# Optimization experiments

Measured on AMD Instinct MI355X. Metric: run time of the kernel, lower is better.

The kernel has to match this reference:

```python
import jax, jax.numpy as jnp
import numpy as np


def _conv1x1(x, w, b):
    # x: (B,C_in,H,W), w: (C_out,C_in), b: (C_out,)
    return jnp.einsum('bchw,oc->bohw', x, w) + b[None, :, None, None]


def _maxpool2x2(x):
    B, C, H, W = x.shape
    return x.reshape(B, C, H // 2, 2, W // 2, 2).max(axis=(3, 5))


def setup_inputs() -> dict:
    key = jax.random.key(0)
    ks = jax.random.split(key, 10)
    B, C, H, W = 16, 64, 64, 64
    d8, d2 = C // 8, C // 2
    s = 0.05
    return {
        'x': jax.random.normal(ks[0], (B, C, H, W), dtype=jnp.float32),
        'w_theta': jax.random.normal(ks[1], (d8, C), dtype=jnp.float32) * s,
        'b_theta': jnp.zeros((d8,), dtype=jnp.float32),
        'w_phi': jax.random.normal(ks[2], (d8, C), dtype=jnp.float32) * s,
        'b_phi': jnp.zeros((d8,), dtype=jnp.float32),
        'w_g': jax.random.normal(ks[3], (d2, C), dtype=jnp.float32) * s,
        'b_g': jnp.zeros((d2,), dtype=jnp.float32),
        'w_o': jax.random.normal(ks[4], (C, d2), dtype=jnp.float32) * s,
        'b_o': jnp.zeros((C,), dtype=jnp.float32),
        'sigma': jnp.ones((1,), dtype=jnp.float32),
    }


def reference(x, w_theta, b_theta, w_phi, b_phi, w_g, b_g, w_o, b_o, sigma):
    B, C, H, W = x.shape
    N = H * W
    theta = _conv1x1(x, w_theta, b_theta).reshape(B, C // 8, N)            # (B, d8, N)
    phi = _maxpool2x2(_conv1x1(x, w_phi, b_phi)).reshape(B, C // 8, N // 4)  # (B, d8, N/4)
    attn = jax.nn.softmax(jnp.einsum('bdn,bdm->bnm', theta, phi), axis=-1)   # (B, N, N/4)
    g = _maxpool2x2(_conv1x1(x, w_g, b_g)).reshape(B, C // 2, N // 4)        # (B, d2, N/4)
    attn_g = jnp.einsum('bcm,bnm->bcn', g, attn).reshape(B, C // 2, H, W)
    attn_g = _conv1x1(attn_g, w_o, b_o)
    return x + sigma[0] * attn_g
```

## Files before the change

kernel.cpp:

```cpp
#include <hip/hip_runtime.h>


#define B_   16
#define C_   64
#define HW_  4096
#define M_   1024

typedef __attribute__((ext_vector_type(8))) short bf16x8;
typedef __attribute__((ext_vector_type(4))) float f32x4;
typedef __attribute__((ext_vector_type(4))) _Float16 f16x4;

#define LOG2E 1.44269504088896340736f

__device__ __forceinline__ unsigned short f2bf(float f) {
    union { float f; unsigned int u; } v; v.f = f;
    return (unsigned short)((v.u + 0x7FFFu + ((v.u >> 16) & 1u)) >> 16);
}
__device__ __forceinline__ unsigned int packh2(float a, float b) {
    auto h = __builtin_amdgcn_cvt_pkrtz(a, b);
    union { decltype(h) h; unsigned int u; } v;
    v.h = h;
    return v.u;
}
__device__ __forceinline__ unsigned int pack2t(float a, float b) {
    union { float f; unsigned int u; } ua, ub; ua.f = a; ub.f = b;
    return (ua.u >> 16) | (ub.u & 0xFFFF0000u);
}

__global__ __launch_bounds__(256) void proj_kernel(
    const float* __restrict__ x,
    const float* __restrict__ w_theta, const float* __restrict__ b_theta,
    const float* __restrict__ w_phi,   const float* __restrict__ b_phi,
    const float* __restrict__ w_g,     const float* __restrict__ b_g,
    unsigned short* __restrict__ thetaH,
    unsigned short* __restrict__ phiH,
    unsigned short* __restrict__ gTp)
{
    __shared__ __align__(16) float x_l[64 * 132];
    __shared__ float pool_l[128][41];

    const int tid = threadIdx.x;
    const int b   = blockIdx.y;
    const int rp  = blockIdx.x;
    const int n0  = rp * 128;

    {
        const float4* src = (const float4*)(x + (size_t)b * C_ * HW_ + n0);
        #pragma unroll
        for (int j = 0; j < 8; j++) {
            int idx = tid + j * 256;
            int c = idx >> 5, p4 = idx & 31;
            float4 v = src[(size_t)c * (HW_ / 4) + p4];
            *(float4*)&x_l[c * 132 + p4 * 4] = v;
        }
    }
    __syncthreads();

    const int px = tid & 127;
    const int og = tid >> 7;

    if (og == 0) {
        float th[8], ph[8], g0[8];
        #pragma unroll
        for (int o = 0; o < 8; o++) { th[o] = b_theta[o]; ph[o] = b_phi[o]; g0[o] = b_g[o]; }
        #pragma unroll 4
        for (int c = 0; c < C_; c++) {
            float xv = x_l[c * 132 + px];
            #pragma unroll
            for (int o = 0; o < 8; o++) th[o] += xv * w_theta[o * 64 + c];
            #pragma unroll
            for (int o = 0; o < 8; o++) ph[o] += xv * w_phi[o * 64 + c];
            #pragma unroll
            for (int o = 0; o < 8; o++) g0[o] += xv * w_g[o * 64 + c];
        }
        unsigned short* tout = thetaH + ((size_t)b * HW_ + n0 + px) * 8;
        uint4 tv;
        tv.x = packh2(th[0] * LOG2E, th[1] * LOG2E);
        tv.y = packh2(th[2] * LOG2E, th[3] * LOG2E);
        tv.z = packh2(th[4] * LOG2E, th[5] * LOG2E);
        tv.w = packh2(th[6] * LOG2E, th[7] * LOG2E);
        *(uint4*)tout = tv;
        #pragma unroll
        for (int o = 0; o < 8; o++) { pool_l[px][o] = ph[o]; pool_l[px][8 + o] = g0[o]; }
    } else {
        float gg[24];
        #pragma unroll
        for (int o = 0; o < 24; o++) gg[o] = b_g[8 + o];
        #pragma unroll 4
        for (int c = 0; c < C_; c++) {
            float xv = x_l[c * 132 + px];
            #pragma unroll
            for (int o = 0; o < 24; o++) gg[o] += xv * w_g[(8 + o) * 64 + c];
        }
        #pragma unroll
        for (int o = 0; o < 24; o++) pool_l[px][16 + o] = gg[o];
    }
    __syncthreads();

    {
        const int j   = tid & 31;
        const int grp = tid >> 5;
        const int p00 = 2 * j, p01 = 2 * j + 1, p10 = 64 + 2 * j, p11 = 65 + 2 * j;
        const int mq   = rp * 32 + j;
        const int pcol = rp * 32 + ((j >> 2) & 3) * 8 + (j >> 4) * 4 + (j & 3);
        #pragma unroll
        for (int k = 0; k < 5; k++) {
            const int ch = grp * 5 + k;
            float v = fmaxf(fmaxf(pool_l[p00][ch], pool_l[p01][ch]),
                            fmaxf(pool_l[p10][ch], pool_l[p11][ch]));
            if (ch < 8)
                ((_Float16*)phiH)[((size_t)b * M_ + mq) * 16 + ch] = (_Float16)v;
            else
                gTp[((size_t)b * 32 + (ch - 8)) * M_ + pcol] = f2bf(v);
        }
        if (tid < 32) {
            *(uint4*)((_Float16*)phiH + ((size_t)b * M_ + rp * 32 + tid) * 16 + 8) =
                make_uint4(0, 0, 0, 0);
        }
    }
}

__global__ __launch_bounds__(256, 4) void attn_kernel(
    const float* __restrict__ x,
    const unsigned short* __restrict__ thetaH,
    const unsigned short* __restrict__ phiH,
    const unsigned short* __restrict__ gTp,
    const float* __restrict__ w_o, const float* __restrict__ b_o,
    const float* __restrict__ sigma,
    float* __restrict__ out)
{
    __shared__ float Op_l[4][32 * 33];
    __shared__ float rs_l[4][32];

    const int tid   = threadIdx.x;
    const int b     = blockIdx.y;
    const int qbase = blockIdx.x * 32;
    const int wv    = tid >> 6;
    const int lane  = tid & 63;
    const int ln15  = lane & 15;
    const int quad  = lane >> 4;

    const _Float16* phiP = (const _Float16*)phiH + (size_t)b * M_ * 16;
    const unsigned short* gP = gTp + (size_t)b * 32 * M_;

    f16x4 th[2];
    {
        const f16x4 z = {0, 0, 0, 0};
        #pragma unroll
        for (int qt = 0; qt < 2; qt++) {
            const _Float16* tp = (const _Float16*)thetaH
                + ((size_t)b * HW_ + qbase + qt * 16 + ln15) * 8 + (quad & 1) * 4;
            f16x4 t = *(const f16x4*)tp;
            th[qt] = (quad < 2) ? t : z;
        }
    }

    #define LD_PHI(ch_, mt_) \
        (*(const f16x4*)(phiP + ((ch_) * 64 + (mt_) * 16 + ln15) * 16 + quad * 4))
    #define LD_G(ch_, h_, s_) \
        (*(const bf16x8*)(gP + (size_t)((h_) * 16 + ln15) * M_ + (ch_) * 64 + (s_) * 32 + quad * 8))

    f16x4 pf[4][4];
    #pragma unroll
    for (int wc = 0; wc < 4; wc++)
        #pragma unroll
        for (int mt = 0; mt < 4; mt++) pf[wc][mt] = LD_PHI(wv * 4 + wc, mt);

    bf16x8 g00 = LD_G(wv * 4, 0, 0), g01 = LD_G(wv * 4, 0, 1);
    bf16x8 g10 = LD_G(wv * 4, 1, 0), g11 = LD_G(wv * 4, 1, 1);

    f32x4 acc[2][2];
    #pragma unroll
    for (int h = 0; h < 2; h++)
        #pragma unroll
        for (int qt = 0; qt < 2; qt++) acc[h][qt] = (f32x4){0.f, 0.f, 0.f, 0.f};
    float rs_p[2] = {0.f, 0.f};

    #pragma unroll
    for (int wc = 0; wc < 4; wc++) {
        bf16x8 n00, n01, n10, n11;
        if (wc < 3) {
            const int nch = wv * 4 + wc + 1;
            n00 = LD_G(nch, 0, 0); n01 = LD_G(nch, 0, 1);
            n10 = LD_G(nch, 1, 0); n11 = LD_G(nch, 1, 1);
        }

        #pragma unroll
        for (int s = 0; s < 2; s++) {
            const bf16x8 gh0 = (s == 0) ? g00 : g01;
            const bf16x8 gh1 = (s == 0) ? g10 : g11;
            #pragma unroll
            for (int qt = 0; qt < 2; qt++) {
                const f32x4 zc = {0.f, 0.f, 0.f, 0.f};
                f32x4 S0 = __builtin_amdgcn_mfma_f32_16x16x16f16(pf[wc][2 * s],     th[qt], zc, 0, 0, 0);
                f32x4 S1 = __builtin_amdgcn_mfma_f32_16x16x16f16(pf[wc][2 * s + 1], th[qt], zc, 0, 0, 0);
                float e0[4], e1[4];
                #pragma unroll
                for (int r = 0; r < 4; r++) {
                    e0[r] = exp2f(S0[r]);
                    e1[r] = exp2f(S1[r]);
                    rs_p[qt] += e0[r] + e1[r];
                }
                union { bf16x8 v; unsigned int u[4]; } pb;
                pb.u[0] = pack2t(e0[0], e0[1]); pb.u[1] = pack2t(e0[2], e0[3]);
                pb.u[2] = pack2t(e1[0], e1[1]); pb.u[3] = pack2t(e1[2], e1[3]);
                acc[0][qt] = __builtin_amdgcn_mfma_f32_16x16x32_bf16(gh0, pb.v, acc[0][qt], 0, 0, 0);
                acc[1][qt] = __builtin_amdgcn_mfma_f32_16x16x32_bf16(gh1, pb.v, acc[1][qt], 0, 0, 0);
            }
        }
        if (wc < 3) { g00 = n00; g01 = n01; g10 = n10; g11 = n11; }
    }
    #undef LD_PHI
    #undef LD_G

    {
        float v[2];
        #pragma unroll
        for (int qt = 0; qt < 2; qt++) {
            float t = rs_p[qt];
            t += __shfl_xor(t, 16);
            t += __shfl_xor(t, 32);
            v[qt] = t;
        }
        if (quad == 0) {
            #pragma unroll
            for (int qt = 0; qt < 2; qt++) rs_l[wv][qt * 16 + ln15] = v[qt];
        }
    }
    #pragma unroll
    for (int h = 0; h < 2; h++)
        #pragma unroll
        for (int qt = 0; qt < 2; qt++)
            #pragma unroll
            for (int r = 0; r < 4; r++)
                Op_l[wv][(qt * 16 + ln15) * 33 + h * 16 + quad * 4 + r] = acc[h][qt][r];
    __syncthreads();

    const int q   = tid & 31;
    const int grp = tid >> 5;
    const float rowsum = rs_l[0][q] + rs_l[1][q] + rs_l[2][q] + rs_l[3][q];
    const float sg  = sigma[0];
    const float inv = sg / rowsum;
    float o[32];
    #pragma unroll
    for (int c = 0; c < 32; c++)
        o[c] = Op_l[0][q * 33 + c] + Op_l[1][q * 33 + c]
             + Op_l[2][q * 33 + c] + Op_l[3][q * 33 + c];
    const size_t xb = (size_t)b * C_ * HW_ + qbase + q;
    #pragma unroll
    for (int k = 0; k < 8; k++) {
        const int co = grp * 8 + k;
        float t = 0.f;
        #pragma unroll
        for (int c = 0; c < 32; c++) t += w_o[co * 32 + c] * o[c];
        out[xb + (size_t)co * HW_] = x[xb + (size_t)co * HW_] + t * inv + sg * b_o[co];
    }
}

extern "C" void kernel_launch(void* const* d_in, const int* in_sizes, int n_in,
                              void* d_out, int out_size, void* d_ws, size_t ws_size,
                              hipStream_t stream)
{
    const float* x       = (const float*)d_in[0];
    const float* w_theta = (const float*)d_in[1];
    const float* b_theta = (const float*)d_in[2];
    const float* w_phi   = (const float*)d_in[3];
    const float* b_phi   = (const float*)d_in[4];
    const float* w_g     = (const float*)d_in[5];
    const float* b_g     = (const float*)d_in[6];
    const float* w_o     = (const float*)d_in[7];
    const float* b_o     = (const float*)d_in[8];
    const float* sigma   = (const float*)d_in[9];
    float* out = (float*)d_out;

    unsigned short* thetaH = (unsigned short*)d_ws;
    unsigned short* phiH   = thetaH + (size_t)B_ * HW_ * 8;
    unsigned short* gTp    = phiH   + (size_t)B_ * M_ * 16;

    proj_kernel<<<dim3(32, B_), 256, 0, stream>>>(
        x, w_theta, b_theta, w_phi, b_phi, w_g, b_g, thetaH, phiH, gTp);
    attn_kernel<<<dim3(128, B_), 256, 0, stream>>>(
        x, thetaH, phiH, gTp, w_o, b_o, sigma, out);
}
```

Measured before the change: 134.2 us.

## Split projection blocks in half and rebalance channel work across four wave groups

After: 131.4 us. 2.0% less time.

```diff
diff --git a/kernel.cpp b/kernel.cpp
--- a/kernel.cpp
+++ b/kernel.cpp
@@ -36,44 +36,47 @@
     unsigned short* __restrict__ phiH,
     unsigned short* __restrict__ gTp)
 {
-    __shared__ __align__(16) float x_l[64 * 132];
-    __shared__ float pool_l[128][41];
+    __shared__ __align__(16) float x_l[64 * 68];
+    __shared__ float pool_l[64][41];
 
     const int tid = threadIdx.x;
     const int b   = blockIdx.y;
-    const int rp  = blockIdx.x;
-    const int n0  = rp * 128;
+    const int rp  = blockIdx.x >> 1;
+    const int hf  = blockIdx.x & 1;
 
     {
-        const float4* src = (const float4*)(x + (size_t)b * C_ * HW_ + n0);
-        #pragma unroll
-        for (int j = 0; j < 8; j++) {
+        const float* src = x + (size_t)b * C_ * HW_ + (size_t)(2 * rp) * 64 + hf * 32;
+        #pragma unroll
+        for (int j = 0; j < 4; j++) {
             int idx = tid + j * 256;
-            int c = idx >> 5, p4 = idx & 31;
-            float4 v = src[(size_t)c * (HW_ / 4) + p4];
-            *(float4*)&x_l[c * 132 + p4 * 4] = v;
+            int c   = idx >> 4, p4 = idx & 15;
+            int row = p4 >> 3,  c4 = p4 & 7;
+            float4 v = *(const float4*)(src + (size_t)c * HW_ + row * 64 + c4 * 4);
+            *(float4*)&x_l[c * 68 + row * 32 + c4 * 4] = v;
         }
     }
     __syncthreads();
 
-    const int px = tid & 127;
-    const int og = tid >> 7;
+    const int px = tid & 63;
+    const int og = tid >> 6;
 
     if (og == 0) {
-        float th[8], ph[8], g0[8];
-        #pragma unroll
-        for (int o = 0; o < 8; o++) { th[o] = b_theta[o]; ph[o] = b_phi[o]; g0[o] = b_g[o]; }
-        #pragma unroll 4
+        float th[8], ph[4];
+        #pragma unroll
+        for (int o = 0; o < 8; o++) th[o] = b_theta[o];
+        #pragma unroll
+        for (int o = 0; o < 4; o++) ph[o] = b_phi[o];
+        #pragma unroll 8
         for (int c = 0; c < C_; c++) {
-            float xv = x_l[c * 132 + px];
+            float xv = x_l[c * 68 + px];
             #pragma unroll
             for (int o = 0; o < 8; o++) th[o] += xv * w_theta[o * 64 + c];
             #pragma unroll
-            for (int o = 0; o < 8; o++) ph[o] += xv * w_phi[o * 64 + c];
-            #pragma unroll
-            for (int o = 0; o < 8; o++) g0[o] += xv * w_g[o * 64 + c];
-        }
-        unsigned short* tout = thetaH + ((size_t)b * HW_ + n0 + px) * 8;
+            for (int o = 0; o < 4; o++) ph[o] += xv * w_phi[o * 64 + c];
+        }
+        const int row = px >> 5, col = px & 31;
+        const int n   = (2 * rp + row) * 64 + hf * 32 + col;
+        unsigned short* tout = thetaH + ((size_t)b * HW_ + n) * 8;
         uint4 tv;
         tv.x = packh2(th[0] * LOG2E, th[1] * LOG2E);
         tv.y = packh2(th[2] * LOG2E, th[3] * LOG2E);
@@ -81,46 +84,77 @@
         tv.w = packh2(th[6] * LOG2E, th[7] * LOG2E);
         *(uint4*)tout = tv;
         #pragma unroll
-        for (int o = 0; o < 8; o++) { pool_l[px][o] = ph[o]; pool_l[px][8 + o] = g0[o]; }
+        for (int o = 0; o < 4; o++) pool_l[px][o] = ph[o];
+    } else if (og == 1) {
+        float ph[4], gg[8];
+        #pragma unroll
+        for (int o = 0; o < 4; o++) ph[o] = b_phi[4 + o];
+        #pragma unroll
+        for (int o = 0; o < 8; o++) gg[o] = b_g[o];
+        #pragma unroll 8
+        for (int c = 0; c < C_; c++) {
+            float xv = x_l[c * 68 + px];
+            #pragma unroll
+            for (int o = 0; o < 4; o++) ph[o] += xv * w_phi[(4 + o) * 64 + c];
+            #pragma unroll
+            for (int o = 0; o < 8; o++) gg[o] += xv * w_g[o * 64 + c];
+        }
+        #pragma unroll
+        for (int o = 0; o < 4; o++) pool_l[px][4 + o] = ph[o];
+        #pragma unroll
+        for (int o = 0; o < 8; o++) pool_l[px][8 + o] = gg[o];
+    } else if (og == 2) {
+        float gg[12];
+        #pragma unroll
+        for (int o = 0; o < 12; o++) gg[o] = b_g[8 + o];
+        #pragma unroll 8
+        for (int c = 0; c < C_; c++) {
+            float xv = x_l[c * 68 + px];
+            #pragma unroll
+            for (int o = 0; o < 12; o++) gg[o] += xv * w_g[(8 + o) * 64 + c];
+        }
+        #pragma unroll
+        for (int o = 0; o < 12; o++) pool_l[px][16 + o] = gg[o];
     } else {
-        float gg[24];
-        #pragma unroll
-        for (int o = 0; o < 24; o++) gg[o] = b_g[8 + o];
-        #pragma unroll 4
+        float gg[12];
+        #pragma unroll
+        for (int o = 0; o < 12; o++) gg[o] = b_g[20 + o];
+        #pragma unroll 8
         for (int c = 0; c < C_; c++) {
-            float xv = x_l[c * 132 + px];
-            #pragma unroll
-            for (int o = 0; o < 24; o++) gg[o] += xv * w_g[(8 + o) * 64 + c];
-        }
-        #pragma unroll
-        for (int o = 0; o < 24; o++) pool_l[px][16 + o] = gg[o];
+            float xv = x_l[c * 68 + px];
+            #pragma unroll
+            for (int o = 0; o < 12; o++) gg[o] += xv * w_g[(20 + o) * 64 + c];
+        }
+        #pragma unroll
+        for (int o = 0; o < 12; o++) pool_l[px][28 + o] = gg[o];
     }
     __syncthreads();
 
     {
-        const int j   = tid & 31;
-        const int grp = tid >> 5;
-        const int p00 = 2 * j, p01 = 2 * j + 1, p10 = 64 + 2 * j, p11 = 65 + 2 * j;
-        const int mq   = rp * 32 + j;
-        const int pcol = rp * 32 + ((j >> 2) & 3) * 8 + (j >> 4) * 4 + (j & 3);
-        #pragma unroll
-        for (int k = 0; k < 5; k++) {
-            const int ch = grp * 5 + k;
-            float v = fmaxf(fmaxf(pool_l[p00][ch], pool_l[p01][ch]),
-                            fmaxf(pool_l[p10][ch], pool_l[p11][ch]));
-            if (ch < 8)
-                ((_Float16*)phiH)[((size_t)b * M_ + mq) * 16 + ch] = (_Float16)v;
-            else
-                gTp[((size_t)b * 32 + (ch - 8)) * M_ + pcol] = f2bf(v);
-        }
-        if (tid < 32) {
-            *(uint4*)((_Float16*)phiH + ((size_t)b * M_ + rp * 32 + tid) * 16 + 8) =
+        const int j = tid & 15, grp = tid >> 4;
+        if (grp < 10) {
+            const int jj   = hf * 16 + j;
+            const int mq   = rp * 32 + jj;
+            const int pcol = rp * 32 + ((jj >> 2) & 3) * 8 + (jj >> 4) * 4 + (jj & 3);
+            #pragma unroll
+            for (int k = 0; k < 4; k++) {
+                const int ch = grp * 4 + k;
+                float v = fmaxf(fmaxf(pool_l[2 * j][ch],      pool_l[2 * j + 1][ch]),
+                                fmaxf(pool_l[32 + 2 * j][ch], pool_l[33 + 2 * j][ch]));
+                if (ch < 8)
+                    ((_Float16*)phiH)[((size_t)b * M_ + mq) * 16 + ch] = (_Float16)v;
+                else
+                    gTp[((size_t)b * 32 + (ch - 8)) * M_ + pcol] = f2bf(v);
+            }
+        }
+        if (tid < 16) {
+            *(uint4*)((_Float16*)phiH + ((size_t)b * M_ + rp * 32 + hf * 16 + tid) * 16 + 8) =
                 make_uint4(0, 0, 0, 0);
         }
     }
 }
 
-__global__ __launch_bounds__(256, 4) void attn_kernel(
+__global__ __launch_bounds__(256, 3) void attn_kernel(
     const float* __restrict__ x,
     const unsigned short* __restrict__ thetaH,
     const unsigned short* __restrict__ phiH,
@@ -277,7 +311,7 @@
     unsigned short* phiH   = thetaH + (size_t)B_ * HW_ * 8;
     unsigned short* gTp    = phiH   + (size_t)B_ * M_ * 16;
 
-    proj_kernel<<<dim3(32, B_), 256, 0, stream>>>(
+    proj_kernel<<<dim3(64, B_), 256, 0, stream>>>(
         x, w_theta, b_theta, w_phi, b_phi, w_g, b_g, thetaH, phiH, gTp);
     attn_kernel<<<dim3(128, B_), 256, 0, stream>>>(
         x, thetaH, phiH, gTp, w_o, b_o, sigma, out);
```
